# Optimization experiments

Hardware: AMD Instinct MI355X
Metric: run time of the kernel (lower is better)

Reference implementation:

```python
import jax, jax.numpy as jnp
import numpy as np

B, S, T, D, H, V, R = 16, 100, 60, 512, 8, 32000, 20
DK = D // H
WIN = 20
DECAY1 = (jnp.arange(WIN, dtype=jnp.float32) + 1.0) / 20.0  # decay1[i] = (i+1)/20


def _add_state_init():
    # decay2[:S] padded with zeros: decay2[i] = 1 - (i+1)/50 for i < 50
    idx = jnp.arange(S, dtype=jnp.float32)
    return jnp.where(idx < 50, 1.0 - (idx + 1.0) / 50.0, 0.0)  # [S]


def _forward(v_outputs, f_outputs, query_seq, attn_logits, Wr, br, Wa, ba, Wq_lin,
             Wn, bn, Wlogit, blogit, Wptr, bptr, Wqr, bqr, Wkr, bkr, src_mask):
    dt = v_outputs.dtype
    add0 = _add_state_init().astype(dt)
    mem0 = v_outputs * add0[None, :, None]                       # [B,S,D]
    add_state0 = jnp.broadcast_to(add0[None, :, None], (B, S, 1)).astype(dt)
    # role_selector keys, computed once (queries change per step)
    k_heads = (f_outputs @ Wkr + bkr).reshape(B, R, H, DK).transpose(0, 2, 1, 3)  # [B,H,R,DK]
    abuf0 = jnp.zeros((WIN, B, S), dt)   # last-20 attn weights (oldest first)
    qbuf0 = jnp.zeros((WIN, B, D), dt)   # last-20 decoder states

    def step(carry, xs):
        mem, add_state, abuf, qbuf, t = carry
        logits_t, q_t = xs               # [B,S], [B,D]
        # masked softmax over frames (uniformed_this in original)
        attn_i = jax.nn.softmax(jnp.where(src_mask, logits_t, -jnp.inf), axis=-1)  # [B,S]
        # memory read: selected_frame = bmm(attn, memory_bank)
        sel = jnp.einsum('bs,bsd->bd', attn_i, mem)
        # role_selector multi-head attention weights (mean over heads)
        qh = (sel @ Wqr + bqr).reshape(B, H, DK)
        scores = jnp.einsum('bhk,bhrk->bhr', qh, k_heads) / jnp.sqrt(jnp.asarray(DK, dt))
        role_attn = jax.nn.softmax(scores, axis=-1).mean(axis=1)  # [B,R]
        # pointer-generator joint distribution
        vocab = q_t @ Wlogit.T + blogit                            # [B,V] (tied embedding)
        p_gen = jax.nn.sigmoid(q_t @ Wptr + bptr)                  # [B,1]
        joint = jnp.concatenate([vocab, role_attn * p_gen], axis=-1)  # [B,V+R]
        # slide 20-step window buffers
        abuf = jnp.concatenate([abuf[1:], attn_i[None]], axis=0)
        qbuf = jnp.concatenate([qbuf[1:], q_t[None]], axis=0)
        # decay-weighted sums: temp = softmax(decay1[20-L:]) over valid window
        L = jnp.minimum(t + 1, WIN)
        w = jax.nn.softmax(jnp.where(jnp.arange(WIN) >= WIN - L, DECAY1, -jnp.inf)).astype(dt)
        attn_w = jnp.einsum('k,kbs->bs', w, abuf)                  # [B,S]
        query_w = jnp.einsum('k,kbd->bd', w, qbuf)                 # [B,D]
        # gated remove
        rem = jax.nn.sigmoid(q_t @ Wr + br)[:, :, None]            # [B,1,1]
        addp = jax.nn.sigmoid(q_t @ Wa + ba)[:, :, None]           # [B,1,1]
        sim = jax.nn.sigmoid(jnp.einsum('bsd,bd->bs', mem, query_w @ Wq_lin.T))[:, :, None]
        mem = mem * (1.0 - rem * attn_w[:, :, None] * sim)
        # gated add
        last_ctx = jnp.einsum('bs,bsd->bd', attn_w, v_outputs)[:, None, :]  # [B,1,D]
        nxt = jax.nn.sigmoid(
            jnp.concatenate([v_outputs, jnp.broadcast_to(last_ctx, (B, S, D))], axis=-1) @ Wn + bn)  # [B,S,1]
        gain = addp * nxt
        mem = mem + v_outputs * (1.0 - add_state) * gain
        add_state = add_state + (1.0 - add_state) * gain
        return (mem, add_state, abuf, qbuf, t + 1), joint

    xs = (attn_logits.transpose(1, 0, 2), query_seq.transpose(1, 0, 2))
    _, joints = jax.lax.scan(step, (mem0, add_state0, abuf0, qbuf0, 0), xs)
    return joints.transpose(1, 0, 2)  # [B,T,V+R]


def setup_inputs() -> dict:
    key = jax.random.key(0)
    ks = jax.random.split(key, 12)
    n = jax.random.normal
    sd = 0.02
    return {
        'v_outputs': n(ks[0], (B, S, D), jnp.float32),
        'f_outputs': n(ks[1], (B, R, D), jnp.float32),
        'query_seq': n(ks[2], (B, T, D), jnp.float32),
        'attn_logits': n(ks[3], (B, T, S), jnp.float32),
        'Wr': n(ks[4], (D, 1), jnp.float32) * sd, 'br': jnp.zeros((1,), jnp.float32),
        'Wa': n(ks[5], (D, 1), jnp.float32) * sd, 'ba': jnp.zeros((1,), jnp.float32),
        'Wq_lin': n(ks[6], (D, D), jnp.float32) * sd,
        'Wn': n(ks[7], (2 * D, 1), jnp.float32) * sd, 'bn': jnp.zeros((1,), jnp.float32),
        'Wlogit': n(ks[8], (V, D), jnp.float32) * sd, 'blogit': jnp.zeros((V,), jnp.float32),
        'Wptr': n(ks[9], (D, 1), jnp.float32) * sd, 'bptr': jnp.zeros((1,), jnp.float32),
        'Wqr': n(ks[10], (D, D), jnp.float32) * sd, 'bqr': jnp.zeros((D,), jnp.float32),
        'Wkr': n(ks[11], (D, D), jnp.float32) * sd, 'bkr': jnp.zeros((D,), jnp.float32),
        'src_mask': jnp.ones((B, S), dtype=bool),
    }


def reference(v_outputs, f_outputs, query_seq, attn_logits, Wr, br, Wa, ba, Wq_lin,
              Wn, bn, Wlogit, blogit, Wptr, bptr, Wqr, bqr, Wkr, bkr, src_mask):
    return _forward(v_outputs, f_outputs, query_seq, attn_logits, Wr, br, Wa, ba, Wq_lin,
                    Wn, bn, Wlogit, blogit, Wptr, bptr, Wqr, bqr, Wkr, bkr, src_mask)
```

## Files before the change

kernel.cpp:

```cpp
#include <hip/hip_runtime.h>
#include <math.h>

constexpr int B = 16, S = 100, T = 60, D = 512, H = 8, V = 32000, R = 20;
constexpr int DK = 64, WIN = 20;
constexpr int VR = V + R;
constexpr int BT = B * T;
constexpr int MP = 1024;
constexpr int TP = 64;
constexpr int FP = 384;

typedef unsigned short u16;
typedef __attribute__((ext_vector_type(8))) short bf16x8;
typedef __attribute__((ext_vector_type(4))) float f32x4;

__device__ __forceinline__ float wred_sum(float v) {
#pragma unroll
  for (int st = 32; st > 0; st >>= 1) v += __shfl_xor(v, st, 64);
  return v;
}
__device__ __forceinline__ float wred_max(float v) {
#pragma unroll
  for (int st = 32; st > 0; st >>= 1) v = fmaxf(v, __shfl_xor(v, st, 64));
  return v;
}
__device__ __forceinline__ float sigmoidf_(float x) { return 1.f / (1.f + expf(-x)); }
__device__ __forceinline__ u16 f2bf(float x) {
  unsigned u = __float_as_uint(x);
  return (u16)((u + 0x7fffu + ((u >> 16) & 1u)) >> 16);
}
__device__ __forceinline__ void gload_lds16(const u16* g, u16* l) {
  __builtin_amdgcn_global_load_lds((const __attribute__((address_space(1))) void*)g,
                                   (__attribute__((address_space(3))) void*)l, 16, 0, 0);
}


__device__ __forceinline__ void vn_body(int row, int l, const float* __restrict__ v,
                                        const float* __restrict__ Wn,
                                        float* __restrict__ vn, float* __restrict__ vn2) {
  const float* vr = v + (size_t)row * D + l * 8;
  float p0 = 0.f, p1 = 0.f;
#pragma unroll
  for (int i = 0; i < 8; i++) {
    float x = vr[i];
    p0 = fmaf(x, Wn[l * 8 + i], p0);
    p1 = fmaf(x, Wn[D + l * 8 + i], p1);
  }
  p0 = wred_sum(p0); p1 = wred_sum(p1);
  if (l == 0) { vn[row] = p0; vn2[row] = p1; }
}

__device__ __forceinline__ void attnscal_body(int row, int l,
    const float* __restrict__ logits, const float* __restrict__ q,
    const float* __restrict__ Wr, const float* __restrict__ br,
    const float* __restrict__ Wa, const float* __restrict__ ba,
    const float* __restrict__ Wptr, const float* __restrict__ bptr,
    float* __restrict__ attn_g, float* __restrict__ remv,
    float* __restrict__ addp, float* __restrict__ pgen) {
  const float* src = logits + (size_t)row * S;
  float a = src[l];
  float b2 = (l + 64 < S) ? src[l + 64] : -INFINITY;
  float m = wred_max(fmaxf(a, b2));
  float ea = expf(a - m), eb = (l + 64 < S) ? expf(b2 - m) : 0.f;
  float inv = 1.f / wred_sum(ea + eb);
  attn_g[(size_t)row * S + l] = ea * inv;
  if (l + 64 < S) attn_g[(size_t)row * S + l + 64] = eb * inv;

  const float* qr = q + (size_t)row * D + l * 8;
  float pr = 0.f, pa = 0.f, pp = 0.f;
#pragma unroll
  for (int i = 0; i < 8; i++) {
    float x = qr[i];
    pr = fmaf(x, Wr[l * 8 + i], pr);
    pa = fmaf(x, Wa[l * 8 + i], pa);
    pp = fmaf(x, Wptr[l * 8 + i], pp);
  }
#pragma unroll
  for (int st = 32; st > 0; st >>= 1) {
    pr += __shfl_xor(pr, st, 64);
    pa += __shfl_xor(pa, st, 64);
    pp += __shfl_xor(pp, st, 64);
  }
  if (l == 0) {
    remv[row] = sigmoidf_(pr + br[0]);
    addp[row] = sigmoidf_(pa + ba[0]);
    pgen[row] = sigmoidf_(pp + bptr[0]);
  }
}

__device__ __forceinline__ void attnw_body(int row, int tid, float* red,
    const float* __restrict__ attn, const float* __restrict__ vn2,
    const float* __restrict__ remv, float* __restrict__ ra, float* __restrict__ ctxn) {
  int b = row / T, t = row % T;
  int L = min(t + 1, WIN);
  if (tid < 128) {
    float dnm = 0.f;
    for (int j = 0; j < L; j++) dnm += expf((float)(WIN - j) / 20.f);
    float p = 0.f;
    if (tid < S) {
      float aw = 0.f;
      for (int j = 0; j < L; j++)
        aw = fmaf(expf((float)(WIN - j) / 20.f) / dnm, attn[(size_t)(row - j) * S + tid], aw);
      ra[(size_t)row * S + tid] = remv[row] * aw;
      p = aw * vn2[b * S + tid];
    }
    red[tid] = p;
  }
  __syncthreads();
  if (tid < 64) {
    float v2 = red[tid] + red[tid + 64];
    v2 = wred_sum(v2);
    if (tid == 0) ctxn[row] = v2;
  }
}

constexpr int NB_CVT = 16960;
constexpr int NB_QWB = MP + 64;
constexpr int NB_PREP = NB_CVT + NB_QWB + 128;
__device__ __forceinline__ void prep_body(int blk, int tid, float (*tile)[65],
    const float* __restrict__ Wlogit, const float* __restrict__ q,
    const float* __restrict__ Wq, const float* __restrict__ f,
    const float* __restrict__ Wqr, const float* __restrict__ Wkr,
    u16* __restrict__ Wlbf, u16* __restrict__ qbf,
    u16* __restrict__ Wqlb, u16* __restrict__ fb,
    u16* __restrict__ qwb, u16* __restrict__ selb,
    u16* __restrict__ WqrT, u16* __restrict__ WkrT) {
  if (blk < NB_CVT) {
    int idx = blk * 256 + tid;
    constexpr int NW = V * D / 4;
    constexpr int NQ = MP * D / 4;
    constexpr int NWQ = D * D / 4;
    if (idx < NW) {
      float4 x = reinterpret_cast<const float4*>(Wlogit)[idx];
      ushort4 o = {f2bf(x.x), f2bf(x.y), f2bf(x.z), f2bf(x.w)};
      reinterpret_cast<ushort4*>(Wlbf)[idx] = o;
    } else if (idx < NW + NQ) {
      int j = idx - NW;
      int row = (j * 4) / D;
      ushort4 o = {0, 0, 0, 0};
      if (row < BT) {
        float4 x = reinterpret_cast<const float4*>(q)[j];
        o = {f2bf(x.x), f2bf(x.y), f2bf(x.z), f2bf(x.w)};
      }
      reinterpret_cast<ushort4*>(qbf)[j] = o;
    } else if (idx < NW + NQ + NWQ) {
      int j = idx - NW - NQ;
      float4 x = reinterpret_cast<const float4*>(Wq)[j];
      ushort4 o = {f2bf(x.x), f2bf(x.y), f2bf(x.z), f2bf(x.w)};
      reinterpret_cast<ushort4*>(Wqlb)[j] = o;
    } else {
      int j = idx - NW - NQ - NWQ;
      int row = (j * 4) / D;
      ushort4 o = {0, 0, 0, 0};
      if (row < B * R) {
        float4 x = reinterpret_cast<const float4*>(f)[j];
        o = {f2bf(x.x), f2bf(x.y), f2bf(x.z), f2bf(x.w)};
      }
      reinterpret_cast<ushort4*>(fb)[j] = o;
    }
  } else if (blk < NB_CVT + NB_QWB) {
    int row = blk - NB_CVT;
    if (row >= MP) {
      size_t base = (size_t)BT * D + (size_t)(row - MP) * D;
      selb[base + tid] = 0; selb[base + tid + 256] = 0;
      return;
    }
    if (row >= BT) {
      qwb[(size_t)row * D + tid] = 0; qwb[(size_t)row * D + tid + 256] = 0;
      return;
    }
    int t = row % T, L = min(t + 1, WIN);
    float dnm = 0.f;
    for (int j = 0; j < L; j++) dnm += expf((float)(WIN - j) / 20.f);
    float a0 = 0.f, a1 = 0.f;
    for (int j = 0; j < L; j++) {
      float wj = expf((float)(WIN - j) / 20.f) / dnm;
      a0 = fmaf(wj, q[(size_t)(row - j) * D + tid], a0);
      a1 = fmaf(wj, q[(size_t)(row - j) * D + tid + 256], a1);
    }
    qwb[(size_t)row * D + tid] = f2bf(a0);
    qwb[(size_t)row * D + tid + 256] = f2bf(a1);
  } else {
    int qt = blk - NB_CVT - NB_QWB;
    const float* src = (qt < 64) ? Wqr : Wkr;
    u16* dst = (qt < 64) ? WqrT : WkrT;
    int q64 = qt & 63;
    int bx = q64 % 8, by = q64 / 8;
#pragma unroll
    for (int i = 0; i < 16; i++) {
      int e = i * 256 + tid, r = e >> 6, c = e & 63;
      tile[r][c] = src[(size_t)(by * 64 + r) * D + bx * 64 + c];
    }
    __syncthreads();
#pragma unroll
    for (int i = 0; i < 16; i++) {
      int e = i * 256 + tid, r = e >> 6, c = e & 63;
      dst[(size_t)(bx * 64 + r) * D + by * 64 + c] = f2bf(tile[c][r]);
    }
  }
}

__device__ __forceinline__ void gemm512_body(const u16* __restrict__ A, const u16* __restrict__ Bw,
                                             const float* __restrict__ bias, float* __restrict__ outp,
                                             int mlimit, int mt, int nt, int tid, u16* ldsbuf) {
  u16* As = ldsbuf;
  u16* Bs = ldsbuf + 128 * 64;
  int m0 = mt * 128, n0 = nt * 128;
  int l = tid & 63;
  int w = tid >> 6, wm = w >> 1, wn = w & 1;
  f32x4 acc[4][4];
#pragma unroll
  for (int mb = 0; mb < 4; mb++)
#pragma unroll
    for (int nb = 0; nb < 4; nb++) acc[mb][nb] = (f32x4){0.f, 0.f, 0.f, 0.f};

  for (int k0 = 0; k0 < D; k0 += 64) {
#pragma unroll
    for (int i = 0; i < 4; i++) {
      int chunk = i * 256 + tid;
      int row = chunk >> 3, kc = chunk & 7;
      int kcs = kc ^ (row & 7);
      gload_lds16(A + (size_t)(m0 + row) * D + k0 + kcs * 8, As + chunk * 8);
      gload_lds16(Bw + (size_t)(n0 + row) * D + k0 + kcs * 8, Bs + chunk * 8);
    }
    __syncthreads();
#pragma unroll
    for (int kk = 0; kk < 2; kk++) {
      bf16x8 af[4], bfr[4];
#pragma unroll
      for (int mb = 0; mb < 4; mb++) {
        int row = wm * 64 + mb * 16 + (l & 15);
        int kc0 = kk * 4 + (l >> 4);
        af[mb] = *(const bf16x8*)(As + row * 64 + ((kc0 ^ (row & 7)) << 3));
      }
#pragma unroll
      for (int nb = 0; nb < 4; nb++) {
        int row = wn * 64 + nb * 16 + (l & 15);
        int kc0 = kk * 4 + (l >> 4);
        bfr[nb] = *(const bf16x8*)(Bs + row * 64 + ((kc0 ^ (row & 7)) << 3));
      }
#pragma unroll
      for (int mb = 0; mb < 4; mb++)
#pragma unroll
        for (int nb = 0; nb < 4; nb++)
          acc[mb][nb] = __builtin_amdgcn_mfma_f32_16x16x32_bf16(af[mb], bfr[nb], acc[mb][nb], 0, 0, 0);
    }
    __syncthreads();
  }

  float* ch = (float*)ldsbuf;
#pragma unroll
  for (int c = 0; c < 4; c++) {
    if (wm == (c >> 1)) {
#pragma unroll
      for (int nb = 0; nb < 4; nb++) {
        int col = wn * 64 + nb * 16 + (l & 15);
        float bl = bias ? bias[n0 + col] : 0.f;
#pragma unroll
        for (int mbi = 0; mbi < 2; mbi++) {
          int mb = (c & 1) * 2 + mbi;
#pragma unroll
          for (int q2 = 0; q2 < 4; q2++) {
            int row_local = mb * 16 + (l >> 4) * 4 + q2 - (c & 1) * 32;
            ch[row_local * 132 + col] = acc[mb][nb][q2] + bl;
          }
        }
      }
    }
    __syncthreads();
#pragma unroll
    for (int p = 0; p < 4; p++) {
      int r = p * 8 + (tid >> 5);
      int m = m0 + c * 32 + r;
      if (m < mlimit) {
        int seg = tid & 31;
        *(float4*)(outp + (size_t)m * D + n0 + seg * 4) =
            *(const float4*)(ch + r * 132 + seg * 4);
      }
    }
    __syncthreads();
  }
}

__device__ __forceinline__ void vocab_body(int bid, int tid, u16* ldsbuf,
    const u16* __restrict__ A, const u16* __restrict__ Bw,
    const float* __restrict__ blog, float* __restrict__ out) {
  u16* As = ldsbuf;
  u16* Bs = ldsbuf + 128 * 64;
  int swz = (bid & 7) * 250 + (bid >> 3);
  int m0 = (swz & 7) * 128, n0 = (swz >> 3) * 128;
  int l = tid & 63;
  int w = tid >> 6, wm = w >> 1, wn = w & 1;

  f32x4 acc[4][4];
#pragma unroll
  for (int mb = 0; mb < 4; mb++)
#pragma unroll
    for (int nb = 0; nb < 4; nb++) acc[mb][nb] = (f32x4){0.f, 0.f, 0.f, 0.f};

  for (int k0 = 0; k0 < D; k0 += 64) {
#pragma unroll
    for (int i = 0; i < 4; i++) {
      int chunk = i * 256 + tid;
      int row = chunk >> 3, kc = chunk & 7;
      int kcs = kc ^ (row & 7);
      gload_lds16(A + (size_t)(m0 + row) * D + k0 + kcs * 8, As + chunk * 8);
      gload_lds16(Bw + (size_t)(n0 + row) * D + k0 + kcs * 8, Bs + chunk * 8);
    }
    __syncthreads();
#pragma unroll
    for (int kk = 0; kk < 2; kk++) {
      bf16x8 af[4], bfr[4];
#pragma unroll
      for (int mb = 0; mb < 4; mb++) {
        int row = wm * 64 + mb * 16 + (l & 15);
        int kc0 = kk * 4 + (l >> 4);
        af[mb] = *(const bf16x8*)(As + row * 64 + ((kc0 ^ (row & 7)) << 3));
      }
#pragma unroll
      for (int nb = 0; nb < 4; nb++) {
        int row = wn * 64 + nb * 16 + (l & 15);
        int kc0 = kk * 4 + (l >> 4);
        bfr[nb] = *(const bf16x8*)(Bs + row * 64 + ((kc0 ^ (row & 7)) << 3));
      }
#pragma unroll
      for (int mb = 0; mb < 4; mb++)
#pragma unroll
        for (int nb = 0; nb < 4; nb++)
          acc[mb][nb] = __builtin_amdgcn_mfma_f32_16x16x32_bf16(af[mb], bfr[nb], acc[mb][nb], 0, 0, 0);
    }
    __syncthreads();
  }

  float* ch = (float*)ldsbuf;
#pragma unroll
  for (int c = 0; c < 4; c++) {
    if (wm == (c >> 1)) {
#pragma unroll
      for (int nb = 0; nb < 4; nb++) {
        int col = wn * 64 + nb * 16 + (l & 15);
        float bl = blog[n0 + col];
#pragma unroll
        for (int mbi = 0; mbi < 2; mbi++) {
          int mb = (c & 1) * 2 + mbi;
#pragma unroll
          for (int q2 = 0; q2 < 4; q2++) {
            int row_local = mb * 16 + (l >> 4) * 4 + q2 - (c & 1) * 32;
            ch[row_local * 132 + col] = acc[mb][nb][q2] + bl;
          }
        }
      }
    }
    __syncthreads();
#pragma unroll
    for (int p = 0; p < 4; p++) {
      int r = p * 8 + (tid >> 5);
      int m = m0 + c * 32 + r;
      if (m < BT) {
        int seg = tid & 31;
        *(float4*)(out + (size_t)m * VR + n0 + seg * 4) =
            *(const float4*)(ch + r * 132 + seg * 4);
      }
    }
    __syncthreads();
  }
}

__device__ __forceinline__ void selgemm_body(int bq, int tid, float* gT ,
    const float* __restrict__ v, const float* __restrict__ gammaT, u16* __restrict__ selb) {
  int b = bq >> 2, dc = bq & 3;
  int dl = tid & 127, th0 = tid >> 7;
  int d = dc * 128 + dl;
  for (int i = tid; i < S * TP; i += 256) {
    int r = i >> 6, c = i & 63;
    gT[r * TP + c] = gammaT[((size_t)b * S + r) * TP + c];
  }
  __syncthreads();
  float acc[2][16];
#pragma unroll
  for (int g = 0; g < 2; g++)
#pragma unroll
    for (int m = 0; m < 16; m++) acc[g][m] = 0.f;
  for (int ss = 0; ss < S; ss++) {
    float vv = v[((size_t)b * S + ss) * D + d];
#pragma unroll
    for (int g = 0; g < 2; g++) {
      int tg = th0 + 2 * g;
      const float* gp = gT + ss * TP + tg * 16;
      float4 g0 = *(const float4*)gp;
      float4 g1 = *(const float4*)(gp + 4);
      float4 g2 = *(const float4*)(gp + 8);
      float4 g3 = *(const float4*)(gp + 12);
      acc[g][0]  = fmaf(g0.x, vv, acc[g][0]);  acc[g][1]  = fmaf(g0.y, vv, acc[g][1]);
      acc[g][2]  = fmaf(g0.z, vv, acc[g][2]);  acc[g][3]  = fmaf(g0.w, vv, acc[g][3]);
      acc[g][4]  = fmaf(g1.x, vv, acc[g][4]);  acc[g][5]  = fmaf(g1.y, vv, acc[g][5]);
      acc[g][6]  = fmaf(g1.z, vv, acc[g][6]);  acc[g][7]  = fmaf(g1.w, vv, acc[g][7]);
      acc[g][8]  = fmaf(g2.x, vv, acc[g][8]);  acc[g][9]  = fmaf(g2.y, vv, acc[g][9]);
      acc[g][10] = fmaf(g2.z, vv, acc[g][10]); acc[g][11] = fmaf(g2.w, vv, acc[g][11]);
      acc[g][12] = fmaf(g3.x, vv, acc[g][12]); acc[g][13] = fmaf(g3.y, vv, acc[g][13]);
      acc[g][14] = fmaf(g3.z, vv, acc[g][14]); acc[g][15] = fmaf(g3.w, vv, acc[g][15]);
    }
  }
#pragma unroll
  for (int g = 0; g < 2; g++) {
    int tg = th0 + 2 * g;
#pragma unroll
    for (int m = 0; m < 16; m++) {
      int t = tg * 16 + m;
      if (t < T) selb[((size_t)b * T + t) * D + d] = f2bf(acc[g][m]);
    }
  }
}

__device__ __forceinline__ void vubeta_body(int bq, int tid, float* sm,
    const float* __restrict__ u, const float* __restrict__ v,
    const float* __restrict__ attn, const float* __restrict__ ra,
    const float* __restrict__ addp, const float* __restrict__ ctxn,
    const float* __restrict__ vn, const float* __restrict__ bn,
    float* __restrict__ gammaT) {
  int b = bq / 5, sc = bq % 5;
  int tq = tid >> 2, sg = tid & 3;
  float* u_s = sm;
  float* v_s = sm + 7920;
  float* aw_s = sm + 10560;
  float* ra_s = sm + 11760;
  float* vu_s = sm + 12960;
  float* gm_s = sm + 14160;
  float* ap_s = sm + 15360;
  float* cx_s = sm + 15420;
  float* vns_s = sm + 15480;
#pragma unroll
  for (int ii = 0; ii < 5; ii++) {
    int i = ii * 256 + tid;
    if (i < T * 20) {
      int t = i / 20, sl = i % 20;
      size_t base = ((size_t)b * T + t) * S + sc * 20 + sl;
      aw_s[t * 20 + sl] = attn[base];
      ra_s[t * 20 + sl] = ra[base];
    }
  }
  if (tid < T) { ap_s[tid] = addp[b * T + tid]; cx_s[tid] = ctxn[b * T + tid]; }
  if (tid >= 64 && tid < 84) vns_s[tid - 64] = vn[b * S + sc * 20 + tid - 64];

  float acc[5] = {0, 0, 0, 0, 0};
  for (int kc = 0; kc < 4; kc++) {
#pragma unroll
    for (int ii = 0; ii < 8; ii++) {
      int i = ii * 256 + tid;
      if (i < 60 * 32) {
        int r = i >> 5, c = (i & 31) * 4;
        *(float4*)&u_s[r * 132 + c] =
            *(const float4*)&u[((size_t)b * T + r) * D + kc * 128 + c];
      }
    }
#pragma unroll
    for (int ii = 0; ii < 3; ii++) {
      int i = ii * 256 + tid;
      if (i < 20 * 32) {
        int r = i >> 5, c = (i & 31) * 4;
        *(float4*)&v_s[r * 132 + c] =
            *(const float4*)&v[((size_t)b * S + sc * 20 + r) * D + kc * 128 + c];
      }
    }
    __syncthreads();
    if (tq < 60) {
#pragma unroll
      for (int e0 = 0; e0 < 128; e0 += 4) {
        float4 uu = *(const float4*)&u_s[tq * 132 + e0];
#pragma unroll
        for (int m = 0; m < 5; m++) {
          float4 vv = *(const float4*)&v_s[(sg * 5 + m) * 132 + e0];
          acc[m] = fmaf(uu.x, vv.x, acc[m]);
          acc[m] = fmaf(uu.y, vv.y, acc[m]);
          acc[m] = fmaf(uu.z, vv.z, acc[m]);
          acc[m] = fmaf(uu.w, vv.w, acc[m]);
        }
      }
    }
    __syncthreads();
  }
  if (tq < 60) {
#pragma unroll
    for (int m = 0; m < 5; m++) vu_s[tq * 20 + sg * 5 + m] = acc[m];
  }
  __syncthreads();
  if (tid < 20) {
    int s = sc * 20 + tid;
    float dec = (s < 50) ? 1.f - (float)(s + 1) / 50.f : 0.f;
    float a = dec, beta = dec;
    float vns = vns_s[tid], bnv = bn[0];
    for (int t = 0; t < T; t++) {
      float g = ap_s[t] * sigmoidf_(vns + cx_s[t] + bnv);
      float wv = (1.f - a) * g;
      a += wv;
      gm_s[t * 20 + tid] = aw_s[t * 20 + tid] * beta;
      beta = beta * (1.f - ra_s[t * 20 + tid] * sigmoidf_(beta * vu_s[t * 20 + tid])) + wv;
    }
  }
  __syncthreads();
#pragma unroll
  for (int ii = 0; ii < 5; ii++) {
    int i = ii * 256 + tid;
    if (i < T * 20) {
      int sl = i / 60, t = i % 60;
      gammaT[((size_t)b * S + sc * 20 + sl) * TP + t] = gm_s[t * 20 + sl];
    }
  }
}


__global__ __launch_bounds__(256) void k_combo1(
    const float* Wlogit, const float* q, const float* Wq, const float* f,
    const float* Wqr, const float* Wkr, const float* logits, const float* v,
    const float* Wn, const float* Wr, const float* br, const float* Wa, const float* ba,
    const float* Wptr, const float* bptr,
    u16* Wlbf, u16* qbf, u16* Wqlb, u16* fb, u16* qwb, u16* selb, u16* WqrT, u16* WkrT,
    float* vn, float* vn2, float* attn_g, float* remv, float* addp, float* pgen) {
  __shared__ float tile[64][65];
  int blk = blockIdx.x, tid = threadIdx.x;
  if (blk < NB_PREP) {
    prep_body(blk, tid, tile, Wlogit, q, Wq, f, Wqr, Wkr,
              Wlbf, qbf, Wqlb, fb, qwb, selb, WqrT, WkrT);
  } else if (blk < NB_PREP + 400) {
    int row = (blk - NB_PREP) * 4 + (tid >> 6);
    vn_body(row, tid & 63, v, Wn, vn, vn2);
  } else {
    int row = (blk - NB_PREP - 400) * 4 + (tid >> 6);
    attnscal_body(row, tid & 63, logits, q, Wr, br, Wa, ba, Wptr, bptr,
                  attn_g, remv, addp, pgen);
  }
}

__global__ __launch_bounds__(256) void k_combo2(
    const u16* qbf, const u16* Wlbf, const float* blog, float* out,
    const u16* qwb, const u16* Wqlb, float* u,
    const u16* fb, const u16* WkrT, const float* bkr, float* khf,
    const float* attn, const float* vn2, const float* remv, float* ra, float* ctxn) {
  __shared__ u16 lds[2 * 128 * 64];
  int blk = blockIdx.x, tid = threadIdx.x;
  if (blk < 600) {
    vocab_body(blk, tid, lds, qbf, Wlbf, blog, out);
  } else if (blk < 644) {
    int z = blk - 600, xx = z % 11, yy = z / 11;
    if (xx < 8) gemm512_body(qwb, Wqlb, nullptr, u, BT, xx, yy, tid, lds);
    else        gemm512_body(fb, WkrT, bkr, khf, B * R, xx - 8, yy, tid, lds);
  } else {
    attnw_body(blk - 644, tid, (float*)lds, attn, vn2, remv, ra, ctxn);
  }
}

__global__ __launch_bounds__(256) void k_vubetap(
    const float* u, const float* v, const float* attn, const float* ra,
    const float* addp, const float* ctxn, const float* vn, const float* bn,
    float* gammaT,
    const u16* qbf, const u16* Wlbf, const float* blog, float* out) {
  __shared__ float smem[15500];
  int blk = blockIdx.x, tid = threadIdx.x;
  if (blk < 80) vubeta_body(blk, tid, smem, u, v, attn, ra, addp, ctxn, vn, bn, gammaT);
  else          vocab_body(600 + blk - 80, tid, (u16*)smem, qbf, Wlbf, blog, out);
}

__global__ __launch_bounds__(256) void k_combo3(
    const u16* qbf, const u16* Wlbf, const float* blog, float* out,
    const float* v, const float* gammaT, u16* selb) {
  __shared__ u16 lds[2 * 128 * 64];
  int blk = blockIdx.x, tid = threadIdx.x;
  if (blk < 600) vocab_body(800 + blk, tid, lds, qbf, Wlbf, blog, out);
  else           selgemm_body(blk - 600, tid, (float*)lds, v, gammaT, selb);
}

__global__ __launch_bounds__(256) void k_combo4(
    const u16* qbf, const u16* Wlbf, const float* blog, float* out,
    const u16* selb, const u16* WqrT, const float* bqr, float* qh) {
  __shared__ u16 lds[2 * 128 * 64];
  int blk = blockIdx.x, tid = threadIdx.x;
  if (blk < 600) vocab_body(1400 + blk, tid, lds, qbf, Wlbf, blog, out);
  else {
    int z = blk - 600;
    gemm512_body(selb, WqrT, bqr, qh, BT, z % 8, z / 8, tid, lds);
  }
}

__global__ void k_role(const float* __restrict__ khf, const float* __restrict__ qh,
                       const float* __restrict__ pgen, float* __restrict__ out) {
  int row = blockIdx.x, tid = threadIdx.x;
  int b = row / T;
  __shared__ float sc[H * R];
  __shared__ float pr[H * R];
  if (tid < H * R) {
    int h = tid / R, r = tid % R;
    const float* qp = qh + (size_t)row * D + h * DK;
    const float* kp = khf + (size_t)(b * R + r) * D + h * DK;
    float acc = 0.f;
#pragma unroll
    for (int i = 0; i < DK; i++) acc = fmaf(qp[i], kp[i], acc);
    sc[tid] = acc * 0.125f;
  }
  __syncthreads();
  if (tid < H) {
    float m = -INFINITY;
    for (int r = 0; r < R; r++) m = fmaxf(m, sc[tid * R + r]);
    float ssum = 0.f;
    for (int r = 0; r < R; r++) { float e = expf(sc[tid * R + r] - m); pr[tid * R + r] = e; ssum += e; }
    float inv = 1.f / ssum;
    for (int r = 0; r < R; r++) pr[tid * R + r] *= inv;
  }
  __syncthreads();
  if (tid < R) {
    float acc = 0.f;
#pragma unroll
    for (int h = 0; h < H; h++) acc += pr[h * R + tid];
    out[(size_t)row * VR + V + tid] = acc * (1.f / H) * pgen[row];
  }
}

extern "C" void kernel_launch(void* const* d_in, const int* in_sizes, int n_in,
                              void* d_out, int out_size, void* d_ws, size_t ws_size,
                              hipStream_t stream) {
  const float* v_out  = (const float*)d_in[0];
  const float* f_out  = (const float*)d_in[1];
  const float* q_seq  = (const float*)d_in[2];
  const float* logits = (const float*)d_in[3];
  const float* Wr     = (const float*)d_in[4];
  const float* br     = (const float*)d_in[5];
  const float* Wa     = (const float*)d_in[6];
  const float* ba     = (const float*)d_in[7];
  const float* Wq_lin = (const float*)d_in[8];
  const float* Wn     = (const float*)d_in[9];
  const float* bn     = (const float*)d_in[10];
  const float* Wlogit = (const float*)d_in[11];
  const float* blogit = (const float*)d_in[12];
  const float* Wptr   = (const float*)d_in[13];
  const float* bptr   = (const float*)d_in[14];
  const float* Wqr    = (const float*)d_in[15];
  const float* bqr    = (const float*)d_in[16];
  const float* Wkr    = (const float*)d_in[17];
  const float* bkr    = (const float*)d_in[18];
  float* out = (float*)d_out;
  float* ws  = (float*)d_ws;

  float* attn   = ws;
  float* ra     = attn   + (size_t)BT * S;
  float* u      = ra     + (size_t)BT * S;
  float* pgen   = u      + (size_t)BT * D;
  float* remv   = pgen   + BT;
  float* addp   = remv   + BT;
  float* ctxn   = addp   + BT;
  float* vn     = ctxn   + BT;
  float* vn2    = vn     + B * S;
  float* khf    = vn2    + B * S;
  float* qh     = khf    + (size_t)B * R * D;
  float* gammaT = qh     + (size_t)BT * D;
  u16*   qwb    = (u16*)(gammaT + (size_t)B * S * TP);
  u16*   selb   = qwb  + (size_t)MP * D;
  u16*   fb     = selb + (size_t)MP * D;
  u16*   Wqlb   = fb   + (size_t)FP * D;
  u16*   WqrT   = Wqlb + (size_t)D * D;
  u16*   WkrT   = WqrT + (size_t)D * D;
  u16*   qbf    = WkrT + (size_t)D * D;
  u16*   Wlbf   = qbf  + (size_t)MP * D;

  k_combo1<<<NB_PREP + 400 + 240, 256, 0, stream>>>(
      Wlogit, q_seq, Wq_lin, f_out, Wqr, Wkr, logits, v_out,
      Wn, Wr, br, Wa, ba, Wptr, bptr,
      Wlbf, qbf, Wqlb, fb, qwb, selb, WqrT, WkrT,
      vn, vn2, attn, remv, addp, pgen);

  k_combo2<<<600 + 44 + 960, 256, 0, stream>>>(
      qbf, Wlbf, blogit, out, qwb, Wqlb, u, fb, WkrT, bkr, khf,
      attn, vn2, remv, ra, ctxn);

  k_vubetap<<<80 + 200, 256, 0, stream>>>(
      u, v_out, attn, ra, addp, ctxn, vn, bn, gammaT, qbf, Wlbf, blogit, out);

  k_combo3<<<600 + B * 4, 256, 0, stream>>>(qbf, Wlbf, blogit, out, v_out, gammaT, selb);

  k_combo4<<<600 + 32, 256, 0, stream>>>(qbf, Wlbf, blogit, out, selb, WqrT, bqr, qh);

  k_role<<<BT, 192, 0, stream>>>(khf, qh, pgen, out);
}
```

Baseline: 181.7 us.

## Reassociate role query projection as gamma·(v·Wqr) and merge role kernel

The role-selector query projection is reassociated. v is first multiplied by Wqr once per batch (a 1600x512x512 bf16 GEMM launched alongside the early vocab tiles), and the gamma-weighted sum over frames then produces qh directly with the bias added. This removes the dependent selb GEMM kernel. The role softmax kernel is merged with the last slice of vocab tiles, and vocab work is rebalanced across the four remaining launches, cutting the launch count from six to five. The cost is an extra v-to-bf16 conversion and a larger GEMM over S=100 frames instead of T=60 steps, which also changes where bf16 rounding happens.

```diff
diff --git a/kernel.cpp b/kernel.cpp
--- a/kernel.cpp
+++ b/kernel.cpp
@@ -8,6 +8,7 @@
 constexpr int MP = 1024;
 constexpr int TP = 64;
 constexpr int FP = 384;
+constexpr int VBP = 1664;
 
 typedef unsigned short u16;
 typedef __attribute__((ext_vector_type(8))) short bf16x8;
@@ -113,22 +114,23 @@
   }
 }
 
-constexpr int NB_CVT = 16960;
-constexpr int NB_QWB = MP + 64;
+constexpr int NW = V * D / 4;
+constexpr int NQ = MP * D / 4;
+constexpr int NWQ = D * D / 4;
+constexpr int NF = FP * D / 4;
+constexpr int NVB = VBP * D / 4;
+constexpr int NB_CVT = (NW + NQ + NWQ + NF + NVB) / 256;
+constexpr int NB_QWB = MP;
 constexpr int NB_PREP = NB_CVT + NB_QWB + 128;
 __device__ __forceinline__ void prep_body(int blk, int tid, float (*tile)[65],
     const float* __restrict__ Wlogit, const float* __restrict__ q,
-    const float* __restrict__ Wq, const float* __restrict__ f,
+    const float* __restrict__ Wq, const float* __restrict__ f, const float* __restrict__ v,
     const float* __restrict__ Wqr, const float* __restrict__ Wkr,
     u16* __restrict__ Wlbf, u16* __restrict__ qbf,
-    u16* __restrict__ Wqlb, u16* __restrict__ fb,
-    u16* __restrict__ qwb, u16* __restrict__ selb,
-    u16* __restrict__ WqrT, u16* __restrict__ WkrT) {
+    u16* __restrict__ Wqlb, u16* __restrict__ fb, u16* __restrict__ vb,
+    u16* __restrict__ qwb, u16* __restrict__ WqrT, u16* __restrict__ WkrT) {
   if (blk < NB_CVT) {
     int idx = blk * 256 + tid;
-    constexpr int NW = V * D / 4;
-    constexpr int NQ = MP * D / 4;
-    constexpr int NWQ = D * D / 4;
     if (idx < NW) {
       float4 x = reinterpret_cast<const float4*>(Wlogit)[idx];
       ushort4 o = {f2bf(x.x), f2bf(x.y), f2bf(x.z), f2bf(x.w)};
@@ -147,7 +149,7 @@
       float4 x = reinterpret_cast<const float4*>(Wq)[j];
       ushort4 o = {f2bf(x.x), f2bf(x.y), f2bf(x.z), f2bf(x.w)};
       reinterpret_cast<ushort4*>(Wqlb)[j] = o;
-    } else {
+    } else if (idx < NW + NQ + NWQ + NF) {
       int j = idx - NW - NQ - NWQ;
       int row = (j * 4) / D;
       ushort4 o = {0, 0, 0, 0};
@@ -156,14 +158,18 @@
         o = {f2bf(x.x), f2bf(x.y), f2bf(x.z), f2bf(x.w)};
       }
       reinterpret_cast<ushort4*>(fb)[j] = o;
+    } else {
+      int j = idx - NW - NQ - NWQ - NF;
+      int row = (j * 4) / D;
+      ushort4 o = {0, 0, 0, 0};
+      if (row < B * S) {
+        float4 x = reinterpret_cast<const float4*>(v)[j];
+        o = {f2bf(x.x), f2bf(x.y), f2bf(x.z), f2bf(x.w)};
+      }
+      reinterpret_cast<ushort4*>(vb)[j] = o;
     }
   } else if (blk < NB_CVT + NB_QWB) {
     int row = blk - NB_CVT;
-    if (row >= MP) {
-      size_t base = (size_t)BT * D + (size_t)(row - MP) * D;
-      selb[base + tid] = 0; selb[base + tid + 256] = 0;
-      return;
-    }
     if (row >= BT) {
       qwb[(size_t)row * D + tid] = 0; qwb[(size_t)row * D + tid + 256] = 0;
       return;
@@ -365,8 +371,9 @@
   }
 }
 
-__device__ __forceinline__ void selgemm_body(int bq, int tid, float* gT ,
-    const float* __restrict__ v, const float* __restrict__ gammaT, u16* __restrict__ selb) {
+__device__ __forceinline__ void qhgemm_body(int bq, int tid, float* gT ,
+    const float* __restrict__ vWqr, const float* __restrict__ gammaT,
+    const float* __restrict__ bqr, float* __restrict__ qh) {
   int b = bq >> 2, dc = bq & 3;
   int dl = tid & 127, th0 = tid >> 7;
   int d = dc * 128 + dl;
@@ -381,7 +388,7 @@
 #pragma unroll
     for (int m = 0; m < 16; m++) acc[g][m] = 0.f;
   for (int ss = 0; ss < S; ss++) {
-    float vv = v[((size_t)b * S + ss) * D + d];
+    float vv = vWqr[((size_t)b * S + ss) * D + d];
 #pragma unroll
     for (int g = 0; g < 2; g++) {
       int tg = th0 + 2 * g;
@@ -400,13 +407,14 @@
       acc[g][14] = fmaf(g3.z, vv, acc[g][14]); acc[g][15] = fmaf(g3.w, vv, acc[g][15]);
     }
   }
+  float bz = bqr[d];
 #pragma unroll
   for (int g = 0; g < 2; g++) {
     int tg = th0 + 2 * g;
 #pragma unroll
     for (int m = 0; m < 16; m++) {
       int t = tg * 16 + m;
-      if (t < T) selb[((size_t)b * T + t) * D + d] = f2bf(acc[g][m]);
+      if (t < T) qh[((size_t)b * T + t) * D + d] = acc[g][m] + bz;
     }
   }
 }
@@ -507,19 +515,50 @@
   }
 }
 
+__device__ __forceinline__ void role_body(int row, int tid, float* sc, float* pr,
+    const float* __restrict__ khf, const float* __restrict__ qh,
+    const float* __restrict__ pgen, float* __restrict__ out) {
+  int b = row / T;
+  if (tid < H * R) {
+    int h = tid / R, r = tid % R;
+    const float* qp = qh + (size_t)row * D + h * DK;
+    const float* kp = khf + (size_t)(b * R + r) * D + h * DK;
+    float acc = 0.f;
+#pragma unroll
+    for (int i = 0; i < DK; i++) acc = fmaf(qp[i], kp[i], acc);
+    sc[tid] = acc * 0.125f;
+  }
+  __syncthreads();
+  if (tid < H) {
+    float m = -INFINITY;
+    for (int r = 0; r < R; r++) m = fmaxf(m, sc[tid * R + r]);
+    float ssum = 0.f;
+    for (int r = 0; r < R; r++) { float e = expf(sc[tid * R + r] - m); pr[tid * R + r] = e; ssum += e; }
+    float inv = 1.f / ssum;
+    for (int r = 0; r < R; r++) pr[tid * R + r] *= inv;
+  }
+  __syncthreads();
+  if (tid < R) {
+    float acc = 0.f;
+#pragma unroll
+    for (int h = 0; h < H; h++) acc += pr[h * R + tid];
+    out[(size_t)row * VR + V + tid] = acc * (1.f / H) * pgen[row];
+  }
+}
+
 
 __global__ __launch_bounds__(256) void k_combo1(
     const float* Wlogit, const float* q, const float* Wq, const float* f,
     const float* Wqr, const float* Wkr, const float* logits, const float* v,
     const float* Wn, const float* Wr, const float* br, const float* Wa, const float* ba,
     const float* Wptr, const float* bptr,
-    u16* Wlbf, u16* qbf, u16* Wqlb, u16* fb, u16* qwb, u16* selb, u16* WqrT, u16* WkrT,
+    u16* Wlbf, u16* qbf, u16* Wqlb, u16* fb, u16* vb, u16* qwb, u16* WqrT, u16* WkrT,
     float* vn, float* vn2, float* attn_g, float* remv, float* addp, float* pgen) {
   __shared__ float tile[64][65];
   int blk = blockIdx.x, tid = threadIdx.x;
   if (blk < NB_PREP) {
-    prep_body(blk, tid, tile, Wlogit, q, Wq, f, Wqr, Wkr,
-              Wlbf, qbf, Wqlb, fb, qwb, selb, WqrT, WkrT);
+    prep_body(blk, tid, tile, Wlogit, q, Wq, f, v, Wqr, Wkr,
+              Wlbf, qbf, Wqlb, fb, vb, qwb, WqrT, WkrT);
   } else if (blk < NB_PREP + 400) {
     int row = (blk - NB_PREP) * 4 + (tid >> 6);
     vn_body(row, tid & 63, v, Wn, vn, vn2);
@@ -534,17 +573,21 @@
     const u16* qbf, const u16* Wlbf, const float* blog, float* out,
     const u16* qwb, const u16* Wqlb, float* u,
     const u16* fb, const u16* WkrT, const float* bkr, float* khf,
+    const u16* vb, const u16* WqrT, float* vWqr,
     const float* attn, const float* vn2, const float* remv, float* ra, float* ctxn) {
   __shared__ u16 lds[2 * 128 * 64];
   int blk = blockIdx.x, tid = threadIdx.x;
-  if (blk < 600) {
+  if (blk < 550) {
     vocab_body(blk, tid, lds, qbf, Wlbf, blog, out);
-  } else if (blk < 644) {
-    int z = blk - 600, xx = z % 11, yy = z / 11;
+  } else if (blk < 594) {
+    int z = blk - 550, xx = z % 11, yy = z / 11;
     if (xx < 8) gemm512_body(qwb, Wqlb, nullptr, u, BT, xx, yy, tid, lds);
     else        gemm512_body(fb, WkrT, bkr, khf, B * R, xx - 8, yy, tid, lds);
+  } else if (blk < 646) {
+    int z = blk - 594;
+    gemm512_body(vb, WqrT, nullptr, vWqr, B * S, z % 13, z / 13, tid, lds);
   } else {
-    attnw_body(blk - 644, tid, (float*)lds, attn, vn2, remv, ra, ctxn);
+    attnw_body(blk - 646, tid, (float*)lds, attn, vn2, remv, ra, ctxn);
   }
 }
 
@@ -556,60 +599,29 @@
   __shared__ float smem[15500];
   int blk = blockIdx.x, tid = threadIdx.x;
   if (blk < 80) vubeta_body(blk, tid, smem, u, v, attn, ra, addp, ctxn, vn, bn, gammaT);
-  else          vocab_body(600 + blk - 80, tid, (u16*)smem, qbf, Wlbf, blog, out);
+  else          vocab_body(550 + blk - 80, tid, (u16*)smem, qbf, Wlbf, blog, out);
 }
 
 __global__ __launch_bounds__(256) void k_combo3(
     const u16* qbf, const u16* Wlbf, const float* blog, float* out,
-    const float* v, const float* gammaT, u16* selb) {
+    const float* vWqr, const float* gammaT, const float* bqr, float* qh) {
   __shared__ u16 lds[2 * 128 * 64];
   int blk = blockIdx.x, tid = threadIdx.x;
-  if (blk < 600) vocab_body(800 + blk, tid, lds, qbf, Wlbf, blog, out);
-  else           selgemm_body(blk - 600, tid, (float*)lds, v, gammaT, selb);
-}
-
-__global__ __launch_bounds__(256) void k_combo4(
-    const u16* qbf, const u16* Wlbf, const float* blog, float* out,
-    const u16* selb, const u16* WqrT, const float* bqr, float* qh) {
+  if (blk < 700) vocab_body(900 + blk, tid, lds, qbf, Wlbf, blog, out);
+  else           qhgemm_body(blk - 700, tid, (float*)lds, vWqr, gammaT, bqr, qh);
+}
+
+__global__ __launch_bounds__(256) void k_rolep(
+    const float* khf, const float* qh, const float* pgen, float* out,
+    const u16* qbf, const u16* Wlbf, const float* blog) {
   __shared__ u16 lds[2 * 128 * 64];
   int blk = blockIdx.x, tid = threadIdx.x;
-  if (blk < 600) vocab_body(1400 + blk, tid, lds, qbf, Wlbf, blog, out);
-  else {
-    int z = blk - 600;
-    gemm512_body(selb, WqrT, bqr, qh, BT, z % 8, z / 8, tid, lds);
-  }
-}
-
-__global__ void k_role(const float* __restrict__ khf, const float* __restrict__ qh,
-                       const float* __restrict__ pgen, float* __restrict__ out) {
-  int row = blockIdx.x, tid = threadIdx.x;
-  int b = row / T;
-  __shared__ float sc[H * R];
-  __shared__ float pr[H * R];
-  if (tid < H * R) {
-    int h = tid / R, r = tid % R;
-    const float* qp = qh + (size_t)row * D + h * DK;
-    const float* kp = khf + (size_t)(b * R + r) * D + h * DK;
-    float acc = 0.f;
-#pragma unroll
-    for (int i = 0; i < DK; i++) acc = fmaf(qp[i], kp[i], acc);
-    sc[tid] = acc * 0.125f;
-  }
-  __syncthreads();
-  if (tid < H) {
-    float m = -INFINITY;
-    for (int r = 0; r < R; r++) m = fmaxf(m, sc[tid * R + r]);
-    float ssum = 0.f;
-    for (int r = 0; r < R; r++) { float e = expf(sc[tid * R + r] - m); pr[tid * R + r] = e; ssum += e; }
-    float inv = 1.f / ssum;
-    for (int r = 0; r < R; r++) pr[tid * R + r] *= inv;
-  }
-  __syncthreads();
-  if (tid < R) {
-    float acc = 0.f;
-#pragma unroll
-    for (int h = 0; h < H; h++) acc += pr[h * R + tid];
-    out[(size_t)row * VR + V + tid] = acc * (1.f / H) * pgen[row];
+  if (blk < 400) {
+    vocab_body(1600 + blk, tid, lds, qbf, Wlbf, blog, out);
+  } else {
+    float* sc = (float*)lds;
+    float* pr = sc + H * R;
+    role_body(blk - 400, tid, sc, pr, khf, qh, pgen, out);
   }
 }
 
@@ -650,9 +662,10 @@
   float* khf    = vn2    + B * S;
   float* qh     = khf    + (size_t)B * R * D;
   float* gammaT = qh     + (size_t)BT * D;
-  u16*   qwb    = (u16*)(gammaT + (size_t)B * S * TP);
-  u16*   selb   = qwb  + (size_t)MP * D;
-  u16*   fb     = selb + (size_t)MP * D;
+  float* vWqr   = gammaT + (size_t)B * S * TP;
+  u16*   qwb    = (u16*)(vWqr + (size_t)B * S * D);
+  u16*   vb     = qwb  + (size_t)MP * D;
+  u16*   fb     = vb   + (size_t)VBP * D;
   u16*   Wqlb   = fb   + (size_t)FP * D;
   u16*   WqrT   = Wqlb + (size_t)D * D;
   u16*   WkrT   = WqrT + (size_t)D * D;
@@ -662,19 +675,17 @@
   k_combo1<<<NB_PREP + 400 + 240, 256, 0, stream>>>(
       Wlogit, q_seq, Wq_lin, f_out, Wqr, Wkr, logits, v_out,
       Wn, Wr, br, Wa, ba, Wptr, bptr,
-      Wlbf, qbf, Wqlb, fb, qwb, selb, WqrT, WkrT,
+      Wlbf, qbf, Wqlb, fb, vb, qwb, WqrT, WkrT,
       vn, vn2, attn, remv, addp, pgen);
 
-  k_combo2<<<600 + 44 + 960, 256, 0, stream>>>(
+  k_combo2<<<550 + 44 + 52 + 960, 256, 0, stream>>>(
       qbf, Wlbf, blogit, out, qwb, Wqlb, u, fb, WkrT, bkr, khf,
-      attn, vn2, remv, ra, ctxn);
-
-  k_vubetap<<<80 + 200, 256, 0, stream>>>(
+      vb, WqrT, vWqr, attn, vn2, remv, ra, ctxn);
+
+  k_vubetap<<<80 + 350, 256, 0, stream>>>(
       u, v_out, attn, ra, addp, ctxn, vn, bn, gammaT, qbf, Wlbf, blogit, out);
 
-  k_combo3<<<600 + B * 4, 256, 0, stream>>>(qbf, Wlbf, blogit, out, v_out, gammaT, selb);
-
-  k_combo4<<<600 + 32, 256, 0, stream>>>(qbf, Wlbf, blogit, out, selb, WqrT, bqr, qh);
-
-  k_role<<<BT, 192, 0, stream>>>(khf, qh, pgen, out);
-}
+  k_combo3<<<700 + B * 4, 256, 0, stream>>>(qbf, Wlbf, blogit, out, vWqr, gammaT, bqr, qh);
+
+  k_rolep<<<400 + BT, 256, 0, stream>>>(khf, qh, pgen, out, qbf, Wlbf, blogit);
+}
```

New measurement: 172.2 us. -5.2%, faster.
